# Kernel optimization log

Hardware: AMD Instinct MI355X
Metric: run time of the kernel (lower is better)

Reference implementation:

```python
import jax, jax.numpy as jnp
from jax import lax
import numpy as np

CONF_THRES = 0.25
IOU_THRES = 0.45
MAX_OUT = 100  # max_output_boxes_per_class
N_BOXES = 25200  # YOLO 640x640 anchor count


def setup_inputs() -> dict:
    key = jax.random.key(0)
    kb, ks = jax.random.split(key)
    u = jax.random.uniform(kb, (N_BOXES, 4), dtype=jnp.float32)
    # build realistic corner boxes (x1,y1,x2,y2) on a 640x640 canvas
    cx, cy = u[:, 0] * 640.0, u[:, 1] * 640.0
    w = u[:, 2] * 60.0 + 4.0
    h = u[:, 3] * 60.0 + 4.0
    boxes = jnp.stack([cx - w / 2, cy - h / 2, cx + w / 2, cy + h / 2], axis=1)
    scores = jax.random.uniform(ks, (N_BOXES,), dtype=jnp.float32)
    return {"boxes": boxes, "scores": scores}


def _nms_indices(boxes, scores):
    """Greedy NMS. Returns (indices[MAX_OUT] into original boxes, valid[MAX_OUT] mask).
    Confidence filtering (scores > conf_thres) is done by masking to -inf so shapes stay static."""
    n = scores.shape[0]
    s = jnp.where(scores > CONF_THRES, scores, -jnp.inf)
    order = jnp.argsort(-s)               # descending score order
    b = boxes[order]                      # [N,4] sorted boxes
    s = s[order]                          # [N] sorted scores
    area = jnp.maximum(b[:, 2] - b[:, 0], 0.0) * jnp.maximum(b[:, 3] - b[:, 1], 0.0)
    pos = jnp.arange(n)

    def body(i, suppressed):
        keep_i = (~suppressed[i]) & jnp.isfinite(s[i])
        lt = jnp.maximum(b[i, :2], b[:, :2])   # intersection top-left
        rb = jnp.minimum(b[i, 2:], b[:, 2:])   # intersection bottom-right
        wh = jnp.maximum(rb - lt, 0.0)
        inter = wh[:, 0] * wh[:, 1]
        iou = inter / (area[i] + area - inter + 1e-9)
        return suppressed | (keep_i & (pos > i) & (iou > IOU_THRES))

    suppressed = lax.fori_loop(0, n, body, jnp.zeros((n,), bool))
    keep = (~suppressed) & jnp.isfinite(s)
    # pack first MAX_OUT kept (already in score order) into fixed-size output
    rank = jnp.cumsum(keep) - 1
    slot = jnp.where(keep & (rank < MAX_OUT), rank, MAX_OUT)  # overflow/dropped -> slot MAX_OUT
    out_idx = jnp.zeros((MAX_OUT + 1,), jnp.int32).at[slot].set(order.astype(jnp.int32))
    out_valid = jnp.zeros((MAX_OUT + 1,), bool).at[slot].set(keep)
    return out_idx[:MAX_OUT], out_valid[:MAX_OUT]


def reference(boxes, scores):
    idx, valid = _nms_indices(boxes, scores)
    vf = valid.astype(boxes.dtype)
    filtered_boxes = boxes[idx] * vf[:, None]   # zero-padded past the kept count
    filtered_scores = scores[idx] * vf
    return filtered_boxes, filtered_scores
```

## Files before the change

### kernel.cpp

```cpp
#include <hip/hip_runtime.h>
#include <math.h>

#define NB      25200
#define NB4     6300
#define THREADS 1024
#define KV      7
#define NBINS   512
#define CAP     128
#define MAXOUT  100
#define CONF    0.25f
#define PRE     0.98f
#define IOU_T   0.45f
#define NWAVE   16
#define ITEMS_FB 25

typedef unsigned long long u64;
typedef unsigned int u32;

__device__ __forceinline__ bool better(float sa_, int ia_, float sb_, int ib_) {
    return (sb_ > sa_) || (sb_ == sa_ && ib_ < ia_);
}

__global__ __launch_bounds__(THREADS, 1)
void nms_all(const float* __restrict__ boxes,
             const float* __restrict__ scores,
             float* __restrict__ out)
{
    const int tid  = threadIdx.x;
    const int lane = tid & 63;
    const int wv   = tid >> 6;

    __shared__ int    hist[NBINS];
    __shared__ u64    keys[CAP];
    __shared__ float4 sbv[CAP];
    __shared__ float  ss[CAP];
    __shared__ float4 cand_b[CAP];
    __shared__ float  cand_s[CAP];
    __shared__ int    cand_i[CAP];
    __shared__ u64    mat[CAP][2];
    __shared__ int    prank[8][CAP];
    __shared__ int    klist[MAXOUT];
    __shared__ int    s_cnt, s_tbin, s_pack, s_kept;
    __shared__ float  red_v[NWAVE];
    __shared__ int    red_i[NWAVE];
    __shared__ float  live[25600];

    const float4* b4 = (const float4*)boxes;
    const float4* s4 = (const float4*)scores;
    const float binscale = (float)NBINS / (1.0f - PRE);

    float4 sc[KV];
#pragma unroll
    for (int k = 0; k < KV; ++k) {
        const int v = k * THREADS + tid;
        sc[k] = (v < NB4) ? s4[v] : make_float4(-1.f, -1.f, -1.f, -1.f);
    }
    if (tid < NBINS) hist[tid] = 0;
    if (tid == 0) { s_cnt = 0; s_pack = 0; }
    __syncthreads();

    int pack = 0;
#pragma unroll
    for (int k = 0; k < KV; ++k) {
        const float el[4] = {sc[k].x, sc[k].y, sc[k].z, sc[k].w};
#pragma unroll
        for (int e = 0; e < 4; ++e) {
            const float s = el[e];
            if (s > CONF) pack += 0x10000;
            if (s > PRE) {
                pack += 1;
                int b = (int)((s - PRE) * binscale);
                b = b < 0 ? 0 : (b > NBINS - 1 ? NBINS - 1 : b);
                atomicAdd(&hist[b], 1);
            }
        }
    }
#pragma unroll
    for (int off = 1; off < 64; off <<= 1) pack += __shfl_xor(pack, off);
    if (lane == 0) atomicAdd(&s_pack, pack);
    __syncthreads();
    const int total_conf = s_pack >> 16;

    if (tid < 64) {
        int h[8], ls[8];
#pragma unroll
        for (int r = 0; r < 8; ++r) h[r] = hist[lane * 8 + r];
        int acc = 0;
#pragma unroll
        for (int r = 7; r >= 0; --r) { acc += h[r]; ls[r] = acc; }
        u32 inc = (u32)acc;
#pragma unroll
        for (int off = 1; off < 64; off <<= 1) {
            const u32 t = __shfl_down(inc, off);
            if (lane + off < 64) inc += t;
        }
        const int excl = (int)inc - acc;
        int loc = NBINS;
#pragma unroll
        for (int r = 7; r >= 0; --r) { if (ls[r] + excl <= CAP) loc = lane * 8 + r; }
#pragma unroll
        for (int off = 32; off >= 1; off >>= 1) {
            const int t = __shfl_xor(loc, off);
            if (t < loc) loc = t;
        }
        if (lane == 0) s_tbin = loc;
    }
    __syncthreads();
    const int tbin = s_tbin;

#pragma unroll
    for (int k = 0; k < KV; ++k) {
        const int v = k * THREADS + tid;
        const float el[4] = {sc[k].x, sc[k].y, sc[k].z, sc[k].w};
#pragma unroll
        for (int e = 0; e < 4; ++e) {
            const float s = el[e];
            bool pred = false;
            if (s > PRE) {
                int b = (int)((s - PRE) * binscale);
                b = b < 0 ? 0 : (b > NBINS - 1 ? NBINS - 1 : b);
                pred = (b >= tbin);
            }
            if (pred) {
                const int pos = atomicAdd(&s_cnt, 1);
                if (pos < CAP) {
                    const int i = 4 * v + e;
                    cand_s[pos] = s; cand_i[pos] = i; cand_b[pos] = b4[i];
                }
            }
        }
    }
    __syncthreads();
    const int M0 = s_cnt;
    const int M  = (M0 > CAP) ? CAP : M0;

    float cs = 0.f; int ci = 0; float4 cb = make_float4(0.f, 0.f, 0.f, 0.f);
    if (tid < CAP) {
        if (tid < M) { cs = cand_s[tid]; ci = cand_i[tid]; cb = cand_b[tid]; }
        keys[tid] = (tid < M)
            ? (((u64)(~__float_as_uint(cs)) << 32) | (u64)(u32)ci)
            : (0xFFFFFFFF00000000ULL | (u64)tid);
    }
    __syncthreads();

    {
        const int key   = tid & (CAP - 1);
        const int chunk = tid >> 7;
        const u64 myk   = keys[key];
        u64 kb[16];
#pragma unroll
        for (int q = 0; q < 16; ++q) kb[q] = keys[chunk * 16 + q];
        int r = 0;
#pragma unroll
        for (int q = 0; q < 16; ++q) r += (kb[q] < myk) ? 1 : 0;
        prank[chunk][key] = r;
    }
    __syncthreads();
    if (tid < CAP && tid < M) {
        int rank = 0;
#pragma unroll
        for (int c = 0; c < 8; ++c) rank += prank[c][tid];
        sbv[rank] = cb;
        ss[rank]  = cs;
    }
    __syncthreads();

    {
        const int word = wv & 1;
        const int rb   = (wv >> 1) * 16;
        const int jidx = (word << 6) + lane;
        const float4 bj = sbv[jidx];
        const float  aj = fmaxf(bj.z - bj.x, 0.f) * fmaxf(bj.w - bj.y, 0.f);
        const bool   jv = (jidx < M);
        for (int ii = 0; ii < 16; ii += 4) {
            float4 bi[4];
#pragma unroll
            for (int q = 0; q < 4; ++q) bi[q] = sbv[rb + ii + q];
#pragma unroll
            for (int q = 0; q < 4; ++q) {
                const int irow = rb + ii + q;
                const float ai = fmaxf(bi[q].z - bi[q].x, 0.f) * fmaxf(bi[q].w - bi[q].y, 0.f);
                const float ltx = fmaxf(bi[q].x, bj.x);
                const float lty = fmaxf(bi[q].y, bj.y);
                const float rbx = fminf(bi[q].z, bj.z);
                const float rby = fminf(bi[q].w, bj.w);
                const float w_ = fmaxf(rbx - ltx, 0.f);
                const float h_ = fmaxf(rby - lty, 0.f);
                const float inter = w_ * h_;
                const float den = ((ai + aj) - inter) + 1e-9f;
                const bool pred = jv && (irow < M) && (jidx > irow) && (inter > IOU_T * den);
                const u64 bal = __ballot(pred);
                if (lane == 0) mat[irow][word] = bal;
            }
        }
    }
    __syncthreads();

    if (tid == 0) {
        u64 r0 = 0, r1 = 0;
        int kept = 0;
        for (int base = 0; base < M && kept < MAXOUT; base += 8) {
            u64 rw[8][2];
#pragma unroll
            for (int q = 0; q < 8; ++q) { rw[q][0] = mat[base + q][0]; rw[q][1] = mat[base + q][1]; }
#pragma unroll
            for (int q = 0; q < 8; ++q) {
                const int i = base + q;
                if (i >= M || kept >= MAXOUT) break;
                const u64 cur = (i < 64) ? r0 : r1;
                if (!((cur >> (i & 63)) & 1ULL)) {
                    klist[kept++] = i;
                    if (kept == MAXOUT) break;
                    r0 |= rw[q][0]; r1 |= rw[q][1];
                }
            }
        }
        s_kept = kept;
    }
    __syncthreads();

    const int kept = s_kept;
    const bool need_fb = (M0 > CAP) || (kept < MAXOUT && M0 < total_conf);
    if (!need_fb) {
        if (tid < MAXOUT) {
            float4 bb = make_float4(0.f, 0.f, 0.f, 0.f);
            float  sc_ = 0.f;
            if (tid < kept) { const int j = klist[tid]; bb = sbv[j]; sc_ = ss[j]; }
            out[4*tid+0] = bb.x; out[4*tid+1] = bb.y;
            out[4*tid+2] = bb.z; out[4*tid+3] = bb.w;
            out[4*MAXOUT + tid] = sc_;
        }
        return;
    }

    if (tid < 25600 - NB) live[NB + tid] = -INFINITY;
    for (int k = 0; k < ITEMS_FB; ++k) {
        const int i = k * THREADS + tid;
        if (i < NB) {
            const float s0 = scores[i];
            live[i] = (s0 > CONF) ? s0 : -INFINITY;
        }
    }
    __syncthreads();
    for (int r = 0; r < MAXOUT; ++r) {
        float lm = -INFINITY; int li = 0x7fffffff;
        for (int k = 0; k < ITEMS_FB; ++k) {
            const int i = k * THREADS + tid;
            const float v = live[i];
            if (v > lm) { lm = v; li = i; }
        }
        float rv = lm; int ri = li;
#pragma unroll
        for (int off = 32; off >= 1; off >>= 1) {
            const float ov = __shfl_xor(rv, off);
            const int   oi = __shfl_xor(ri, off);
            if (better(rv, ri, ov, oi)) { rv = ov; ri = oi; }
        }
        __syncthreads();
        if (lane == 0) { red_v[wv] = rv; red_i[wv] = ri; }
        __syncthreads();
        float wval = red_v[0]; int widx = red_i[0];
#pragma unroll
        for (int j = 1; j < NWAVE; ++j) {
            const float v = red_v[j]; const int i2 = red_i[j];
            if (better(wval, widx, v, i2)) { wval = v; widx = i2; }
        }
        if (!(wval > -1e38f)) {
            if (tid == 0) {
                out[4*r+0]=0.f; out[4*r+1]=0.f; out[4*r+2]=0.f; out[4*r+3]=0.f;
                out[4*MAXOUT + r] = 0.f;
            }
            continue;
        }
        const float4 wb = b4[widx];
        if (tid == 0) {
            out[4*r+0]=wb.x; out[4*r+1]=wb.y; out[4*r+2]=wb.z; out[4*r+3]=wb.w;
            out[4*MAXOUT + r] = wval;
        }
        const float warea = fmaxf(wb.z - wb.x, 0.f) * fmaxf(wb.w - wb.y, 0.f);
        for (int k = 0; k < ITEMS_FB; ++k) {
            const int i = k * THREADS + tid;
            if (i < NB) {
                const float4 bb = b4[i];
                const float area = fmaxf(bb.z - bb.x, 0.f) * fmaxf(bb.w - bb.y, 0.f);
                const float ltx = fmaxf(bb.x, wb.x);
                const float lty = fmaxf(bb.y, wb.y);
                const float rbx = fminf(bb.z, wb.z);
                const float rby = fminf(bb.w, wb.w);
                const float w  = fmaxf(rbx - ltx, 0.f);
                const float h  = fmaxf(rby - lty, 0.f);
                const float inter = w * h;
                const float den = ((warea + area) - inter) + 1e-9f;
                if (inter > IOU_T * den || i == widx) live[i] = -INFINITY;
            }
        }
        __syncthreads();
    }
}

extern "C" void kernel_launch(void* const* d_in, const int* in_sizes, int n_in,
                              void* d_out, int out_size, void* d_ws, size_t ws_size,
                              hipStream_t stream) {
    const float* boxes  = (const float*)d_in[0];
    const float* scores = (const float*)d_in[1];
    float* out = (float*)d_out;
    nms_all<<<dim3(1), dim3(THREADS), 0, stream>>>(boxes, scores, out);
}
```

Before: 77.19 us.

## Parallelize greedy suppression scan across a wavefront and move fallback buffer to workspace

The serial single-thread walk over the 128x128 suppression bitmask is replaced by a wavefront-wide scan. Each lane owns two candidate rows and uses ballot/shfl to find the next alive leader and broadcast its suppression row. The 100KB shared `live` array used only by the fallback path moves to global workspace, which shrinks LDS use. The score/box output store is also vectorized to float4. The fallback path now uses slower global memory, and the wave loop pays shuffle latency per kept box.

```diff
diff --git a/kernel.cpp b/kernel.cpp
--- a/kernel.cpp
+++ b/kernel.cpp
@@ -24,7 +24,8 @@
 __global__ __launch_bounds__(THREADS, 1)
 void nms_all(const float* __restrict__ boxes,
              const float* __restrict__ scores,
-             float* __restrict__ out)
+             float* __restrict__ out,
+             float* __restrict__ ws_live)
 {
     const int tid  = threadIdx.x;
     const int lane = tid & 63;
@@ -43,7 +44,6 @@
     __shared__ int    s_cnt, s_tbin, s_pack, s_kept;
     __shared__ float  red_v[NWAVE];
     __shared__ int    red_i[NWAVE];
-    __shared__ float  live[25600];
 
     const float4* b4 = (const float4*)boxes;
     const float4* s4 = (const float4*)scores;
@@ -196,26 +196,31 @@
     }
     __syncthreads();
 
-    if (tid == 0) {
-        u64 r0 = 0, r1 = 0;
+    if (wv == 0) {
+        const int r0i = 2 * lane, r1i = 2 * lane + 1;
+        const u64 m00 = mat[r0i][0], m01 = mat[r0i][1];
+        const u64 m10 = mat[r1i][0], m11 = mat[r1i][1];
+        u32 alive = ((r0i < M) ? 1u : 0u) | ((r1i < M) ? 2u : 0u);
         int kept = 0;
-        for (int base = 0; base < M && kept < MAXOUT; base += 8) {
-            u64 rw[8][2];
-#pragma unroll
-            for (int q = 0; q < 8; ++q) { rw[q][0] = mat[base + q][0]; rw[q][1] = mat[base + q][1]; }
-#pragma unroll
-            for (int q = 0; q < 8; ++q) {
-                const int i = base + q;
-                if (i >= M || kept >= MAXOUT) break;
-                const u64 cur = (i < 64) ? r0 : r1;
-                if (!((cur >> (i & 63)) & 1ULL)) {
-                    klist[kept++] = i;
-                    if (kept == MAXOUT) break;
-                    r0 |= rw[q][0]; r1 |= rw[q][1];
-                }
-            }
-        }
-        s_kept = kept;
+        while (kept < MAXOUT) {
+            const u64 bal = __ballot(alive != 0u);
+            if (!bal) break;
+            const int ldr = __ffsll(bal) - 1;
+            const u32 la  = __shfl(alive, ldr);
+            const int sub = (la & 1u) ? 0 : 1;
+            const int row = 2 * ldr + sub;
+            const u64 ra  = __shfl(sub ? m10 : m00, ldr);
+            const u64 rb  = __shfl(sub ? m11 : m01, ldr);
+            if (lane == 0) klist[kept] = row;
+            ++kept;
+            if (kept == MAXOUT) break;
+            u32 kill = 0;
+            kill |= (u32)(((r0i < 64) ? (ra >> r0i) : (rb >> (r0i - 64))) & 1ULL);
+            kill |= (u32)(((r1i < 64) ? (ra >> r1i) : (rb >> (r1i - 64))) & 1ULL) << 1;
+            alive &= ~kill;
+            if (lane == ldr) alive &= ~(1u << sub);
+        }
+        if (lane == 0) s_kept = kept;
     }
     __syncthreads();
 
@@ -226,19 +231,18 @@
             float4 bb = make_float4(0.f, 0.f, 0.f, 0.f);
             float  sc_ = 0.f;
             if (tid < kept) { const int j = klist[tid]; bb = sbv[j]; sc_ = ss[j]; }
-            out[4*tid+0] = bb.x; out[4*tid+1] = bb.y;
-            out[4*tid+2] = bb.z; out[4*tid+3] = bb.w;
+            ((float4*)out)[tid] = bb;
             out[4*MAXOUT + tid] = sc_;
         }
         return;
     }
 
-    if (tid < 25600 - NB) live[NB + tid] = -INFINITY;
+    if (tid < 25600 - NB) ws_live[NB + tid] = -INFINITY;
     for (int k = 0; k < ITEMS_FB; ++k) {
         const int i = k * THREADS + tid;
         if (i < NB) {
             const float s0 = scores[i];
-            live[i] = (s0 > CONF) ? s0 : -INFINITY;
+            ws_live[i] = (s0 > CONF) ? s0 : -INFINITY;
         }
     }
     __syncthreads();
@@ -246,7 +250,7 @@
         float lm = -INFINITY; int li = 0x7fffffff;
         for (int k = 0; k < ITEMS_FB; ++k) {
             const int i = k * THREADS + tid;
-            const float v = live[i];
+            const float v = ws_live[i];
             if (v > lm) { lm = v; li = i; }
         }
         float rv = lm; int ri = li;
@@ -291,7 +295,7 @@
                 const float h  = fmaxf(rby - lty, 0.f);
                 const float inter = w * h;
                 const float den = ((warea + area) - inter) + 1e-9f;
-                if (inter > IOU_T * den || i == widx) live[i] = -INFINITY;
+                if (inter > IOU_T * den || i == widx) ws_live[i] = -INFINITY;
             }
         }
         __syncthreads();
@@ -304,5 +308,5 @@
     const float* boxes  = (const float*)d_in[0];
     const float* scores = (const float*)d_in[1];
     float* out = (float*)d_out;
-    nms_all<<<dim3(1), dim3(THREADS), 0, stream>>>(boxes, scores, out);
+    nms_all<<<dim3(1), dim3(THREADS), 0, stream>>>(boxes, scores, out, (float*)d_ws);
 }
```

After: 83.71 us, median of 2. +8.4%, slower.
